# Performance work log

Measured on AMD Instinct MI355X. Metric: run time of the kernel, lower is better.

The kernel has to match this reference:

```python
import jax, jax.numpy as jnp
import numpy as np

B = 16384
NUM_RATE, NUM_GENRE, NUM_DIRECTOR, NUM_ACTOR = 6, 25, 2186, 8030
EMB = 32


def setup_inputs() -> dict:
    key = jax.random.key(0)
    k0, k1, k2, k3, k4 = jax.random.split(key, 5)
    x = jax.random.randint(k0, (B, 1 + NUM_GENRE + NUM_DIRECTOR + NUM_ACTOR), 0, 2, dtype=jnp.int64 if jax.config.jax_enable_x64 else jnp.int32)
    rate_table = jax.random.normal(k1, (NUM_RATE, EMB), dtype=jnp.float32)
    # torch Linear weights have shape [out_features, in_features]
    W_genre = jax.random.normal(k2, (EMB, NUM_GENRE), dtype=jnp.float32) * (1.0 / np.sqrt(NUM_GENRE))
    W_director = jax.random.normal(k3, (EMB, NUM_DIRECTOR), dtype=jnp.float32) * (1.0 / np.sqrt(NUM_DIRECTOR))
    W_actor = jax.random.normal(k4, (EMB, NUM_ACTOR), dtype=jnp.float32) * (1.0 / np.sqrt(NUM_ACTOR))
    return {"x": x, "rate_table": rate_table, "W_genre": W_genre,
            "W_director": W_director, "W_actor": W_actor}


def _maxnorm_gather(table, idx, max_norm=1.0, eps=1e-7):
    # torch.nn.Embedding(max_norm=1.0): rows accessed are renormalized to norm <= max_norm
    rows = table[idx]  # [B, E]
    norm = jnp.linalg.norm(rows, axis=-1, keepdims=True)
    scale = jnp.where(norm > max_norm, max_norm / (norm + eps), 1.0)
    return rows * scale


def _mean_pool_linear(multi_hot_f, W):
    # Linear(no bias) on multi-hot then divide by row-sum == mean-pooled embedding bag
    emb = jnp.einsum('bn,en->be', multi_hot_f, W)
    return emb / jnp.sum(multi_hot_f, axis=1, keepdims=True)


def reference(x, rate_table, W_genre, W_director, W_actor):
    rate_idx = x[:, 0]
    genre = x[:, 1:26].astype(jnp.float32)
    director = x[:, 26:2212].astype(jnp.float32)
    actors = x[:, 2212:10242].astype(jnp.float32)
    rate_emb = _maxnorm_gather(rate_table, rate_idx)
    genre_emb = _mean_pool_linear(genre, W_genre)
    director_emb = _mean_pool_linear(director, W_director)
    actors_emb = _mean_pool_linear(actors, W_actor)
    return jnp.concatenate((rate_emb, genre_emb, director_emb, actors_emb), axis=1)  # [B, 4*EMB]
```

## Files before the change

kernel.cpp:

```cpp
#include <hip/hip_runtime.h>
#include <hip/hip_bf16.h>

#define B_ROWS 16384
#define XC     10242
#define NGENRE 25
#define NDIR   2186
#define NACT   8030
#define EMB    32
#define KT_TOTAL 321
#define OUTC   128
#define NCOLS  112
#define PART_STRIDE ((size_t)B_ROWS * NCOLS)

typedef __attribute__((ext_vector_type(8))) short bf16x8;
typedef __attribute__((ext_vector_type(4), aligned(4))) float f32x4a;
typedef __attribute__((ext_vector_type(4))) float f32x4;
typedef __attribute__((ext_vector_type(8))) unsigned short u16x8;

__device__ __forceinline__ void compute_core(
    const int* __restrict__ xrow, int t, int ktA, int ktB,
    const float* __restrict__ wg, const float* __restrict__ wd,
    const float* __restrict__ wa, unsigned short* __restrict__ ldsA,
    f32x4& accG0, f32x4& accG1, f32x4& accD0, f32x4& accD1,
    f32x4& accA0, f32x4& accA1, f32x4& accI) {
  const int srow = t >> 2;
  const int kg   = (t & 3) * 8;
  const int lane = t & 63;
  const int w    = t >> 6;
  const int lo   = lane & 15, hi = lane >> 4;

  auto load_x8 = [&](int kt, int* dst) {
    int k0 = kt * 32 + kg;
    if (k0 + 7 < XC) {
      int4 a = *reinterpret_cast<const int4*>(xrow + k0);
      int4 b = *reinterpret_cast<const int4*>(xrow + k0 + 4);
      dst[0]=a.x; dst[1]=a.y; dst[2]=a.z; dst[3]=a.w;
      dst[4]=b.x; dst[5]=b.y; dst[6]=b.z; dst[7]=b.w;
    } else {
#pragma unroll
      for (int i = 0; i < 8; ++i) dst[i] = (k0 + i < XC) ? xrow[k0 + i] : 0;
    }
  };
  auto bfbits = [](float f) -> unsigned short {
    __hip_bfloat16 h = __float2bfloat16(f);
    return *reinterpret_cast<unsigned short*>(&h);
  };
  auto wval = [&](const float* base, int elem, bool inb) -> unsigned short {
    return inb ? bfbits(base[elem]) : (unsigned short)0;
  };
  auto fragv = [&](const float* base, int elem) -> bf16x8 {
    f32x4a a = *reinterpret_cast<const f32x4a*>(base + elem);
    f32x4a c = *reinterpret_cast<const f32x4a*>(base + elem + 4);
    union { unsigned short u[8]; bf16x8 v; } cv;
#pragma unroll
    for (int j = 0; j < 4; ++j) { cv.u[j] = bfbits(a[j]); cv.u[j+4] = bfbits(c[j]); }
    return cv.v;
  };
  auto pack8 = [](const unsigned short* s) -> bf16x8 {
    union { unsigned short u[8]; bf16x8 v; } cv;
#pragma unroll
    for (int i = 0; i < 8; ++i) cv.u[i] = s[i];
    return cv.v;
  };

  int xv[2][8];
  load_x8(ktA, xv[0]);
  if (ktA + 1 < ktB) load_x8(ktA + 1, xv[1]);

  for (int kt = ktA; kt < ktB; ++kt) {
    int* cx = xv[kt & 1];
    unsigned short cur[8];
#pragma unroll
    for (int i = 0; i < 8; ++i)
      cur[i] = cx[i] ? (unsigned short)0x3F80 : (unsigned short)0;
    if (kt + 2 < ktB) load_x8(kt + 2, xv[kt & 1]);

    __syncthreads();
    *reinterpret_cast<u16x8*>(&ldsA[srow * 40 + kg]) =
        *reinterpret_cast<const u16x8*>(cur);
    __syncthreads();

    bf16x8 afrag = *reinterpret_cast<const bf16x8*>(&ldsA[(w * 16 + lo) * 40 + hi * 8]);
    const int kb = kt * 32 + hi * 8;

    {
      unsigned short iv[8];
#pragma unroll
      for (int j = 0; j < 8; ++j) {
        int k = kb + j;
        bool on = (lo == 0) ? (k >= 1 && k < 26)
                : (lo == 1) ? (k >= 26 && k < 2212)
                : (lo == 2) ? (k >= 2212 && k < XC)
                : false;
        iv[j] = on ? (unsigned short)0x3F80 : (unsigned short)0;
      }
      accI = __builtin_amdgcn_mfma_f32_16x16x32_bf16(afrag, pack8(iv), accI, 0, 0, 0);
    }

    if (kt == 0) {
      unsigned short g0[8], g1[8], d0[8], d1[8];
#pragma unroll
      for (int j = 0; j < 8; ++j) {
        int k = kb + j;
        bool ing = (k >= 1 && k < 26);
        bool ind = (k >= 26);
        g0[j] = wval(wg, lo * NGENRE + (k - 1), ing);
        g1[j] = wval(wg, (16 + lo) * NGENRE + (k - 1), ing);
        d0[j] = wval(wd, lo * NDIR + (k - 26), ind);
        d1[j] = wval(wd, (16 + lo) * NDIR + (k - 26), ind);
      }
      accG0 = __builtin_amdgcn_mfma_f32_16x16x32_bf16(afrag, pack8(g0), accG0, 0, 0, 0);
      accG1 = __builtin_amdgcn_mfma_f32_16x16x32_bf16(afrag, pack8(g1), accG1, 0, 0, 0);
      accD0 = __builtin_amdgcn_mfma_f32_16x16x32_bf16(afrag, pack8(d0), accD0, 0, 0, 0);
      accD1 = __builtin_amdgcn_mfma_f32_16x16x32_bf16(afrag, pack8(d1), accD1, 0, 0, 0);
    } else if (kt < 69) {
      int e0 = lo * NDIR + kb - 26, e1 = (16 + lo) * NDIR + kb - 26;
      bf16x8 b0 = fragv(wd, e0), b1 = fragv(wd, e1);
      accD0 = __builtin_amdgcn_mfma_f32_16x16x32_bf16(afrag, b0, accD0, 0, 0, 0);
      accD1 = __builtin_amdgcn_mfma_f32_16x16x32_bf16(afrag, b1, accD1, 0, 0, 0);
    } else if (kt == 69) {
      unsigned short d0[8], d1[8], a0[8], a1[8];
#pragma unroll
      for (int j = 0; j < 8; ++j) {
        int k = kb + j;
        bool ind = (k < 2212);
        d0[j] = wval(wd, lo * NDIR + (k - 26), ind);
        d1[j] = wval(wd, (16 + lo) * NDIR + (k - 26), ind);
        a0[j] = wval(wa, lo * NACT + (k - 2212), !ind);
        a1[j] = wval(wa, (16 + lo) * NACT + (k - 2212), !ind);
      }
      accD0 = __builtin_amdgcn_mfma_f32_16x16x32_bf16(afrag, pack8(d0), accD0, 0, 0, 0);
      accD1 = __builtin_amdgcn_mfma_f32_16x16x32_bf16(afrag, pack8(d1), accD1, 0, 0, 0);
      accA0 = __builtin_amdgcn_mfma_f32_16x16x32_bf16(afrag, pack8(a0), accA0, 0, 0, 0);
      accA1 = __builtin_amdgcn_mfma_f32_16x16x32_bf16(afrag, pack8(a1), accA1, 0, 0, 0);
    } else if (kt < 320) {
      int e0 = lo * NACT + kb - 2212, e1 = (16 + lo) * NACT + kb - 2212;
      bf16x8 b0 = fragv(wa, e0), b1 = fragv(wa, e1);
      accA0 = __builtin_amdgcn_mfma_f32_16x16x32_bf16(afrag, b0, accA0, 0, 0, 0);
      accA1 = __builtin_amdgcn_mfma_f32_16x16x32_bf16(afrag, b1, accA1, 0, 0, 0);
    } else {
      unsigned short a0[8], a1[8];
#pragma unroll
      for (int j = 0; j < 8; ++j) {
        int k = kb + j;
        bool in = (k < XC);
        a0[j] = wval(wa, lo * NACT + (k - 2212), in);
        a1[j] = wval(wa, (16 + lo) * NACT + (k - 2212), in);
      }
      accA0 = __builtin_amdgcn_mfma_f32_16x16x32_bf16(afrag, pack8(a0), accA0, 0, 0, 0);
      accA1 = __builtin_amdgcn_mfma_f32_16x16x32_bf16(afrag, pack8(a1), accA1, 0, 0, 0);
    }
  }
}

template<int KS>
__global__ __launch_bounds__(256) void main_mm(const int* __restrict__ x,
                                               const float* __restrict__ wg,
                                               const float* __restrict__ wd,
                                               const float* __restrict__ wa,
                                               float* __restrict__ part) {
  __shared__ unsigned short ldsA[64 * 40];
  constexpr int PER = (KT_TOTAL + KS - 1) / KS;

  const int t  = threadIdx.x;
  const int rb = blockIdx.x & 255;
  const int ks = blockIdx.x >> 8;
  const int ktA = ks * PER;
  const int ktB = (ktA + PER < KT_TOTAL) ? ktA + PER : KT_TOTAL;
  const int* xrow = x + (size_t)(rb * 64 + (t >> 2)) * XC;

  f32x4 accG0 = {0,0,0,0}, accG1 = {0,0,0,0};
  f32x4 accD0 = {0,0,0,0}, accD1 = {0,0,0,0};
  f32x4 accA0 = {0,0,0,0}, accA1 = {0,0,0,0};
  f32x4 accI  = {0,0,0,0};

  compute_core(xrow, t, ktA, ktB, wg, wd, wa, ldsA,
               accG0, accG1, accD0, accD1, accA0, accA1, accI);

  const int lane = t & 63;
  const int lo = lane & 15, hi = lane >> 4, w = t >> 6;
  float* slab = part + (size_t)ks * PART_STRIDE;
  const int rbase = rb * 64 + w * 16 + hi * 4;
#pragma unroll
  for (int j = 0; j < 4; ++j) {
    size_t ro = (size_t)(rbase + j) * NCOLS;
    slab[ro +  0 + lo] = accG0[j];
    slab[ro + 16 + lo] = accG1[j];
    slab[ro + 32 + lo] = accD0[j];
    slab[ro + 48 + lo] = accD1[j];
    slab[ro + 64 + lo] = accA0[j];
    slab[ro + 80 + lo] = accA1[j];
    if (lo < 3) slab[ro + 96 + lo] = accI[j];
  }
}

__global__ __launch_bounds__(128) void reduce_k(const int* __restrict__ x,
                                                const float* __restrict__ rate,
                                                const float* __restrict__ part,
                                                int ksplit,
                                                float* __restrict__ out) {
  __shared__ float cnt[3];
  const int r = blockIdx.x;
  const int c = threadIdx.x;

  if (c < 3) {
    float s = 0.f;
    for (int ks = 0; ks < ksplit; ++ks)
      s += part[(size_t)ks * PART_STRIDE + (size_t)r * NCOLS + 96 + c];
    cnt[c] = s;
  }
  __syncthreads();

  float res;
  if (c < EMB) {
    int idx = x[(size_t)r * XC];
    float v = rate[idx * EMB + c];
    float s2 = v * v;
    s2 += __shfl_xor(s2, 1, 32);
    s2 += __shfl_xor(s2, 2, 32);
    s2 += __shfl_xor(s2, 4, 32);
    s2 += __shfl_xor(s2, 8, 32);
    s2 += __shfl_xor(s2, 16, 32);
    float norm = sqrtf(s2);
    float scale = (norm > 1.0f) ? (1.0f / (norm + 1e-7f)) : 1.0f;
    res = v * scale;
  } else {
    int cc = c - EMB;
    float val = 0.f;
    for (int ks = 0; ks < ksplit; ++ks)
      val += part[(size_t)ks * PART_STRIDE + (size_t)r * NCOLS + cc];
    res = val / cnt[cc >> 5];
  }
  out[(size_t)r * OUTC + c] = res;
}

__global__ __launch_bounds__(256) void fused_k(const int* __restrict__ x,
                                               const float* __restrict__ rate,
                                               const float* __restrict__ wg,
                                               const float* __restrict__ wd,
                                               const float* __restrict__ wa,
                                               float* __restrict__ out) {
  __shared__ unsigned short ldsA[64 * 40];
  const int t  = threadIdx.x;
  const int rb = blockIdx.x;
  const int* xrow = x + (size_t)(rb * 64 + (t >> 2)) * XC;

  f32x4 accG0 = {0,0,0,0}, accG1 = {0,0,0,0};
  f32x4 accD0 = {0,0,0,0}, accD1 = {0,0,0,0};
  f32x4 accA0 = {0,0,0,0}, accA1 = {0,0,0,0};
  f32x4 accI  = {0,0,0,0};

  compute_core(xrow, t, 0, KT_TOTAL, wg, wd, wa, ldsA,
               accG0, accG1, accD0, accD1, accA0, accA1, accI);

  const int lane = t & 63;
  const int lo = lane & 15, hi = lane >> 4, w = t >> 6;
  float gc[4], dc[4], ac[4];
#pragma unroll
  for (int j = 0; j < 4; ++j) {
    gc[j] = __shfl(accI[j], (lane & 48));
    dc[j] = __shfl(accI[j], (lane & 48) | 1);
    ac[j] = __shfl(accI[j], (lane & 48) | 2);
  }
  const int rbase = rb * 64 + w * 16 + hi * 4;
#pragma unroll
  for (int j = 0; j < 4; ++j) {
    size_t ro = (size_t)(rbase + j) * OUTC;
    out[ro +  32 + lo] = accG0[j] / gc[j];
    out[ro +  48 + lo] = accG1[j] / gc[j];
    out[ro +  64 + lo] = accD0[j] / dc[j];
    out[ro +  80 + lo] = accD1[j] / dc[j];
    out[ro +  96 + lo] = accA0[j] / ac[j];
    out[ro + 112 + lo] = accA1[j] / ac[j];
  }
#pragma unroll
  for (int j = 0; j < 4; ++j) {
    int row = rbase + j;
    int idx = x[(size_t)row * XC];
    float v0 = rate[idx * EMB + 2 * lo];
    float v1 = rate[idx * EMB + 2 * lo + 1];
    float s2 = v0 * v0 + v1 * v1;
    s2 += __shfl_xor(s2, 1);
    s2 += __shfl_xor(s2, 2);
    s2 += __shfl_xor(s2, 4);
    s2 += __shfl_xor(s2, 8);
    float norm = sqrtf(s2);
    float scale = (norm > 1.0f) ? (1.0f / (norm + 1e-7f)) : 1.0f;
    reinterpret_cast<float2*>(out)[(size_t)row * 64 + lo] =
        make_float2(v0 * scale, v1 * scale);
  }
}

extern "C" void kernel_launch(void* const* d_in, const int* in_sizes, int n_in,
                              void* d_out, int out_size, void* d_ws, size_t ws_size,
                              hipStream_t stream) {
  (void)in_sizes; (void)n_in; (void)out_size;
  const int*   x    = (const int*)d_in[0];
  const float* rate = (const float*)d_in[1];
  const float* wg   = (const float*)d_in[2];
  const float* wd   = (const float*)d_in[3];
  const float* wa   = (const float*)d_in[4];
  float* out  = (float*)d_out;
  float* part = (float*)d_ws;

  const size_t slab_bytes = PART_STRIDE * sizeof(float);
  if (ws_size >= 8 * slab_bytes) {
    main_mm<8><<<8 * 256, 256, 0, stream>>>(x, wg, wd, wa, part);
    reduce_k<<<B_ROWS, 128, 0, stream>>>(x, rate, part, 8, out);
  } else if (ws_size >= 4 * slab_bytes) {
    main_mm<4><<<4 * 256, 256, 0, stream>>>(x, wg, wd, wa, part);
    reduce_k<<<B_ROWS, 128, 0, stream>>>(x, rate, part, 4, out);
  } else if (ws_size >= 2 * slab_bytes) {
    main_mm<2><<<2 * 256, 256, 0, stream>>>(x, wg, wd, wa, part);
    reduce_k<<<B_ROWS, 128, 0, stream>>>(x, rate, part, 2, out);
  } else {
    fused_k<<<256, 256, 0, stream>>>(x, rate, wg, wd, wa, out);
  }
}
```

Before: 1.053 ms.

## Pre-pack bf16 weight fragments and load x directly into MFMA A-fragments

Adds a prep kernel that converts the fp32 weight matrices once per call into bf16 MFMA B-fragment layout in workspace, so the main loop does a single 16-byte load per fragment instead of strided fp32 loads plus conversion. Each lane now loads its own x row segment and builds the A fragment in registers, removing the LDS staging and both __syncthreads per k-tile. The count-column constants are precomputed outside the loop. This costs an extra launch and workspace, and the x loads become less coalesced per wavefront.

```diff
diff --git a/kernel.cpp b/kernel.cpp
--- a/kernel.cpp
+++ b/kernel.cpp
@@ -11,174 +11,156 @@
 #define OUTC   128
 #define NCOLS  112
 #define PART_STRIDE ((size_t)B_ROWS * NCOLS)
-
-typedef __attribute__((ext_vector_type(8))) short bf16x8;
-typedef __attribute__((ext_vector_type(4), aligned(4))) float f32x4a;
-typedef __attribute__((ext_vector_type(4))) float f32x4;
-typedef __attribute__((ext_vector_type(8))) unsigned short u16x8;
-
-__device__ __forceinline__ void compute_core(
-    const int* __restrict__ xrow, int t, int ktA, int ktB,
-    const float* __restrict__ wg, const float* __restrict__ wd,
-    const float* __restrict__ wa, unsigned short* __restrict__ ldsA,
-    f32x4& accG0, f32x4& accG1, f32x4& accD0, f32x4& accD1,
-    f32x4& accA0, f32x4& accA1, f32x4& accI) {
-  const int srow = t >> 2;
-  const int kg   = (t & 3) * 8;
+#define WFRAG_BYTES ((size_t)KT_TOTAL * 4 * 64 * 16)
+
+typedef short bf16x8 __attribute__((ext_vector_type(8)));
+typedef float f32x4  __attribute__((ext_vector_type(4)));
+typedef int   i32x4a __attribute__((ext_vector_type(4), aligned(4)));
+
+__global__ void prep_wfrag(const float* __restrict__ wg,
+                           const float* __restrict__ wd,
+                           const float* __restrict__ wa,
+                           uint4* __restrict__ Wfrag) {
+  const int kt = blockIdx.x;
+  const int s  = threadIdx.x >> 6;
+  const int l  = threadIdx.x & 63;
+  const int n  = l & 15;
+  const int k0 = kt * 32 + ((l >> 4) << 3);
+
+  unsigned short v[8];
+#pragma unroll
+  for (int j = 0; j < 8; ++j) {
+    const int k = k0 + j;
+    float f = 0.f;
+    if (kt == 0) {
+      if (s < 2) { if (k >= 1 && k < 26) f = wg[(s * 16 + n) * NGENRE + (k - 1)]; }
+      else       { if (k >= 26)          f = wd[((s - 2) * 16 + n) * NDIR + (k - 26)]; }
+    } else if (kt < 69) {
+      if (s < 2) f = wd[(s * 16 + n) * NDIR + (k - 26)];
+    } else if (kt == 69) {
+      if (s < 2) { if (k < 2212)  f = wd[(s * 16 + n) * NDIR + (k - 26)]; }
+      else       { if (k >= 2212) f = wa[((s - 2) * 16 + n) * NACT + (k - 2212)]; }
+    } else if (kt < 320) {
+      if (s < 2) f = wa[(s * 16 + n) * NACT + (k - 2212)];
+    } else {
+      if (s < 2 && k < XC) f = wa[(s * 16 + n) * NACT + (k - 2212)];
+    }
+    __hip_bfloat16 h = __float2bfloat16(f);
+    v[j] = *reinterpret_cast<unsigned short*>(&h);
+  }
+  union { unsigned short u[8]; uint4 q; } cv;
+#pragma unroll
+  for (int j = 0; j < 8; ++j) cv.u[j] = v[j];
+  Wfrag[((size_t)kt * 4 + s) * 64 + l] = cv.q;
+}
+
+template<int KS>
+__global__ __launch_bounds__(256) void main_mm(const int* __restrict__ x,
+                                               const uint4* __restrict__ Wfrag,
+                                               float* __restrict__ part) {
+  constexpr int PER = (KT_TOTAL + KS - 1) / KS;
+  const int t    = threadIdx.x;
+  const int rb   = blockIdx.x & 255;
+  const int ks   = blockIdx.x >> 8;
+  const int ktA  = ks * PER;
+  const int ktB  = (ktA + PER < KT_TOTAL) ? ktA + PER : KT_TOTAL;
   const int lane = t & 63;
   const int w    = t >> 6;
   const int lo   = lane & 15, hi = lane >> 4;
-
-  auto load_x8 = [&](int kt, int* dst) {
-    int k0 = kt * 32 + kg;
-    if (k0 + 7 < XC) {
-      int4 a = *reinterpret_cast<const int4*>(xrow + k0);
-      int4 b = *reinterpret_cast<const int4*>(xrow + k0 + 4);
-      dst[0]=a.x; dst[1]=a.y; dst[2]=a.z; dst[3]=a.w;
-      dst[4]=b.x; dst[5]=b.y; dst[6]=b.z; dst[7]=b.w;
-    } else {
-#pragma unroll
-      for (int i = 0; i < 8; ++i) dst[i] = (k0 + i < XC) ? xrow[k0 + i] : 0;
-    }
-  };
-  auto bfbits = [](float f) -> unsigned short {
-    __hip_bfloat16 h = __float2bfloat16(f);
-    return *reinterpret_cast<unsigned short*>(&h);
-  };
-  auto wval = [&](const float* base, int elem, bool inb) -> unsigned short {
-    return inb ? bfbits(base[elem]) : (unsigned short)0;
-  };
-  auto fragv = [&](const float* base, int elem) -> bf16x8 {
-    f32x4a a = *reinterpret_cast<const f32x4a*>(base + elem);
-    f32x4a c = *reinterpret_cast<const f32x4a*>(base + elem + 4);
-    union { unsigned short u[8]; bf16x8 v; } cv;
-#pragma unroll
-    for (int j = 0; j < 4; ++j) { cv.u[j] = bfbits(a[j]); cv.u[j+4] = bfbits(c[j]); }
-    return cv.v;
-  };
-  auto pack8 = [](const unsigned short* s) -> bf16x8 {
-    union { unsigned short u[8]; bf16x8 v; } cv;
-#pragma unroll
-    for (int i = 0; i < 8; ++i) cv.u[i] = s[i];
-    return cv.v;
-  };
-
-  int xv[2][8];
-  load_x8(ktA, xv[0]);
-  if (ktA + 1 < ktB) load_x8(ktA + 1, xv[1]);
-
-  for (int kt = ktA; kt < ktB; ++kt) {
-    int* cx = xv[kt & 1];
-    unsigned short cur[8];
-#pragma unroll
-    for (int i = 0; i < 8; ++i)
-      cur[i] = cx[i] ? (unsigned short)0x3F80 : (unsigned short)0;
-    if (kt + 2 < ktB) load_x8(kt + 2, xv[kt & 1]);
-
-    __syncthreads();
-    *reinterpret_cast<u16x8*>(&ldsA[srow * 40 + kg]) =
-        *reinterpret_cast<const u16x8*>(cur);
-    __syncthreads();
-
-    bf16x8 afrag = *reinterpret_cast<const bf16x8*>(&ldsA[(w * 16 + lo) * 40 + hi * 8]);
-    const int kb = kt * 32 + hi * 8;
-
-    {
-      unsigned short iv[8];
-#pragma unroll
-      for (int j = 0; j < 8; ++j) {
-        int k = kb + j;
-        bool on = (lo == 0) ? (k >= 1 && k < 26)
-                : (lo == 1) ? (k >= 26 && k < 2212)
-                : (lo == 2) ? (k >= 2212 && k < XC)
-                : false;
-        iv[j] = on ? (unsigned short)0x3F80 : (unsigned short)0;
-      }
-      accI = __builtin_amdgcn_mfma_f32_16x16x32_bf16(afrag, pack8(iv), accI, 0, 0, 0);
-    }
-
-    if (kt == 0) {
-      unsigned short g0[8], g1[8], d0[8], d1[8];
-#pragma unroll
-      for (int j = 0; j < 8; ++j) {
-        int k = kb + j;
-        bool ing = (k >= 1 && k < 26);
-        bool ind = (k >= 26);
-        g0[j] = wval(wg, lo * NGENRE + (k - 1), ing);
-        g1[j] = wval(wg, (16 + lo) * NGENRE + (k - 1), ing);
-        d0[j] = wval(wd, lo * NDIR + (k - 26), ind);
-        d1[j] = wval(wd, (16 + lo) * NDIR + (k - 26), ind);
-      }
-      accG0 = __builtin_amdgcn_mfma_f32_16x16x32_bf16(afrag, pack8(g0), accG0, 0, 0, 0);
-      accG1 = __builtin_amdgcn_mfma_f32_16x16x32_bf16(afrag, pack8(g1), accG1, 0, 0, 0);
-      accD0 = __builtin_amdgcn_mfma_f32_16x16x32_bf16(afrag, pack8(d0), accD0, 0, 0, 0);
-      accD1 = __builtin_amdgcn_mfma_f32_16x16x32_bf16(afrag, pack8(d1), accD1, 0, 0, 0);
-    } else if (kt < 69) {
-      int e0 = lo * NDIR + kb - 26, e1 = (16 + lo) * NDIR + kb - 26;
-      bf16x8 b0 = fragv(wd, e0), b1 = fragv(wd, e1);
-      accD0 = __builtin_amdgcn_mfma_f32_16x16x32_bf16(afrag, b0, accD0, 0, 0, 0);
-      accD1 = __builtin_amdgcn_mfma_f32_16x16x32_bf16(afrag, b1, accD1, 0, 0, 0);
-    } else if (kt == 69) {
-      unsigned short d0[8], d1[8], a0[8], a1[8];
-#pragma unroll
-      for (int j = 0; j < 8; ++j) {
-        int k = kb + j;
-        bool ind = (k < 2212);
-        d0[j] = wval(wd, lo * NDIR + (k - 26), ind);
-        d1[j] = wval(wd, (16 + lo) * NDIR + (k - 26), ind);
-        a0[j] = wval(wa, lo * NACT + (k - 2212), !ind);
-        a1[j] = wval(wa, (16 + lo) * NACT + (k - 2212), !ind);
-      }
-      accD0 = __builtin_amdgcn_mfma_f32_16x16x32_bf16(afrag, pack8(d0), accD0, 0, 0, 0);
-      accD1 = __builtin_amdgcn_mfma_f32_16x16x32_bf16(afrag, pack8(d1), accD1, 0, 0, 0);
-      accA0 = __builtin_amdgcn_mfma_f32_16x16x32_bf16(afrag, pack8(a0), accA0, 0, 0, 0);
-      accA1 = __builtin_amdgcn_mfma_f32_16x16x32_bf16(afrag, pack8(a1), accA1, 0, 0, 0);
-    } else if (kt < 320) {
-      int e0 = lo * NACT + kb - 2212, e1 = (16 + lo) * NACT + kb - 2212;
-      bf16x8 b0 = fragv(wa, e0), b1 = fragv(wa, e1);
-      accA0 = __builtin_amdgcn_mfma_f32_16x16x32_bf16(afrag, b0, accA0, 0, 0, 0);
-      accA1 = __builtin_amdgcn_mfma_f32_16x16x32_bf16(afrag, b1, accA1, 0, 0, 0);
-    } else {
-      unsigned short a0[8], a1[8];
-#pragma unroll
-      for (int j = 0; j < 8; ++j) {
-        int k = kb + j;
-        bool in = (k < XC);
-        a0[j] = wval(wa, lo * NACT + (k - 2212), in);
-        a1[j] = wval(wa, (16 + lo) * NACT + (k - 2212), in);
-      }
-      accA0 = __builtin_amdgcn_mfma_f32_16x16x32_bf16(afrag, pack8(a0), accA0, 0, 0, 0);
-      accA1 = __builtin_amdgcn_mfma_f32_16x16x32_bf16(afrag, pack8(a1), accA1, 0, 0, 0);
-    }
-  }
-}
-
-template<int KS>
-__global__ __launch_bounds__(256) void main_mm(const int* __restrict__ x,
-                                               const float* __restrict__ wg,
-                                               const float* __restrict__ wd,
-                                               const float* __restrict__ wa,
-                                               float* __restrict__ part) {
-  __shared__ unsigned short ldsA[64 * 40];
-  constexpr int PER = (KT_TOTAL + KS - 1) / KS;
-
-  const int t  = threadIdx.x;
-  const int rb = blockIdx.x & 255;
-  const int ks = blockIdx.x >> 8;
-  const int ktA = ks * PER;
-  const int ktB = (ktA + PER < KT_TOTAL) ? ktA + PER : KT_TOTAL;
-  const int* xrow = x + (size_t)(rb * 64 + (t >> 2)) * XC;
+  const int* xrow = x + (size_t)(rb * 64 + w * 16 + lo) * XC;
 
   f32x4 accG0 = {0,0,0,0}, accG1 = {0,0,0,0};
   f32x4 accD0 = {0,0,0,0}, accD1 = {0,0,0,0};
   f32x4 accA0 = {0,0,0,0}, accA1 = {0,0,0,0};
   f32x4 accI  = {0,0,0,0};
 
-  compute_core(xrow, t, ktA, ktB, wg, wd, wa, ldsA,
-               accG0, accG1, accD0, accD1, accA0, accA1, accI);
-
-  const int lane = t & 63;
-  const int lo = lane & 15, hi = lane >> 4, w = t >> 6;
+  auto load_x8 = [&](int kt, int* dst) {
+    int k0 = kt * 32 + hi * 8;
+    if (k0 + 7 < XC) {
+      i32x4a a = *reinterpret_cast<const i32x4a*>(xrow + k0);
+      i32x4a b = *reinterpret_cast<const i32x4a*>(xrow + k0 + 4);
+      dst[0]=a[0]; dst[1]=a[1]; dst[2]=a[2]; dst[3]=a[3];
+      dst[4]=b[0]; dst[5]=b[1]; dst[6]=b[2]; dst[7]=b[3];
+    } else {
+#pragma unroll
+      for (int j = 0; j < 8; ++j) dst[j] = (k0 + j < XC) ? xrow[k0 + j] : 0;
+    }
+  };
+  auto bload = [&](int kt, int s) -> bf16x8 {
+    union { uint4 q; bf16x8 v; } c;
+    c.q = Wfrag[((size_t)kt * 4 + s) * 64 + lane];
+    return c.v;
+  };
+  auto mkconst = [&](bool on) -> bf16x8 {
+    union { unsigned int w[4]; bf16x8 v; } c;
+    unsigned int u = on ? 0x3F803F80u : 0u;
+    c.w[0]=u; c.w[1]=u; c.w[2]=u; c.w[3]=u;
+    return c.v;
+  };
+  const bf16x8 ivD = mkconst(lo == 1);
+  const bf16x8 ivA = mkconst(lo == 2);
+
+  int xv[2][8];
+  load_x8(ktA, xv[0]);
+  if (ktA + 1 < ktB) load_x8(ktA + 1, xv[1]);
+
+  for (int kt = ktA; kt < ktB; ++kt) {
+    int* cx = xv[kt & 1];
+    union { unsigned int w[4]; bf16x8 v; } af;
+#pragma unroll
+    for (int i = 0; i < 4; ++i)
+      af.w[i] = (cx[2*i] ? 0x3F80u : 0u) | (cx[2*i+1] ? 0x3F800000u : 0u);
+    if (kt + 2 < ktB) load_x8(kt + 2, xv[kt & 1]);
+    const bf16x8 a = af.v;
+    const int kb = kt * 32 + hi * 8;
+
+    if (kt == 0) {
+      accG0 = __builtin_amdgcn_mfma_f32_16x16x32_bf16(a, bload(0,0), accG0, 0,0,0);
+      accG1 = __builtin_amdgcn_mfma_f32_16x16x32_bf16(a, bload(0,1), accG1, 0,0,0);
+      accD0 = __builtin_amdgcn_mfma_f32_16x16x32_bf16(a, bload(0,2), accD0, 0,0,0);
+      accD1 = __builtin_amdgcn_mfma_f32_16x16x32_bf16(a, bload(0,3), accD1, 0,0,0);
+      union { unsigned short u[8]; bf16x8 v; } iv;
+#pragma unroll
+      for (int j = 0; j < 8; ++j) {
+        int k = kb + j;
+        bool on = (lo == 0) ? (k >= 1 && k < 26) : (lo == 1) ? (k >= 26) : false;
+        iv.u[j] = on ? (unsigned short)0x3F80 : (unsigned short)0;
+      }
+      accI = __builtin_amdgcn_mfma_f32_16x16x32_bf16(a, iv.v, accI, 0,0,0);
+    } else if (kt < 69) {
+      accD0 = __builtin_amdgcn_mfma_f32_16x16x32_bf16(a, bload(kt,0), accD0, 0,0,0);
+      accD1 = __builtin_amdgcn_mfma_f32_16x16x32_bf16(a, bload(kt,1), accD1, 0,0,0);
+      accI  = __builtin_amdgcn_mfma_f32_16x16x32_bf16(a, ivD, accI, 0,0,0);
+    } else if (kt == 69) {
+      accD0 = __builtin_amdgcn_mfma_f32_16x16x32_bf16(a, bload(69,0), accD0, 0,0,0);
+      accD1 = __builtin_amdgcn_mfma_f32_16x16x32_bf16(a, bload(69,1), accD1, 0,0,0);
+      accA0 = __builtin_amdgcn_mfma_f32_16x16x32_bf16(a, bload(69,2), accA0, 0,0,0);
+      accA1 = __builtin_amdgcn_mfma_f32_16x16x32_bf16(a, bload(69,3), accA1, 0,0,0);
+      union { unsigned short u[8]; bf16x8 v; } iv;
+#pragma unroll
+      for (int j = 0; j < 8; ++j) {
+        int k = kb + j;
+        bool on = (lo == 1) ? (k < 2212) : (lo == 2) ? (k >= 2212) : false;
+        iv.u[j] = on ? (unsigned short)0x3F80 : (unsigned short)0;
+      }
+      accI = __builtin_amdgcn_mfma_f32_16x16x32_bf16(a, iv.v, accI, 0,0,0);
+    } else if (kt < 320) {
+      accA0 = __builtin_amdgcn_mfma_f32_16x16x32_bf16(a, bload(kt,0), accA0, 0,0,0);
+      accA1 = __builtin_amdgcn_mfma_f32_16x16x32_bf16(a, bload(kt,1), accA1, 0,0,0);
+      accI  = __builtin_amdgcn_mfma_f32_16x16x32_bf16(a, ivA, accI, 0,0,0);
+    } else {
+      accA0 = __builtin_amdgcn_mfma_f32_16x16x32_bf16(a, bload(320,0), accA0, 0,0,0);
+      accA1 = __builtin_amdgcn_mfma_f32_16x16x32_bf16(a, bload(320,1), accA1, 0,0,0);
+      union { unsigned short u[8]; bf16x8 v; } iv;
+#pragma unroll
+      for (int j = 0; j < 8; ++j) {
+        int k = kb + j;
+        iv.u[j] = (lo == 2 && k < XC) ? (unsigned short)0x3F80 : (unsigned short)0;
+      }
+      accI = __builtin_amdgcn_mfma_f32_16x16x32_bf16(a, iv.v, accI, 0,0,0);
+    }
+  }
+
   float* slab = part + (size_t)ks * PART_STRIDE;
   const int rbase = rb * 64 + w * 16 + hi * 4;
 #pragma unroll
@@ -234,63 +216,6 @@
   out[(size_t)r * OUTC + c] = res;
 }
 
-__global__ __launch_bounds__(256) void fused_k(const int* __restrict__ x,
-                                               const float* __restrict__ rate,
-                                               const float* __restrict__ wg,
-                                               const float* __restrict__ wd,
-                                               const float* __restrict__ wa,
-                                               float* __restrict__ out) {
-  __shared__ unsigned short ldsA[64 * 40];
-  const int t  = threadIdx.x;
-  const int rb = blockIdx.x;
-  const int* xrow = x + (size_t)(rb * 64 + (t >> 2)) * XC;
-
-  f32x4 accG0 = {0,0,0,0}, accG1 = {0,0,0,0};
-  f32x4 accD0 = {0,0,0,0}, accD1 = {0,0,0,0};
-  f32x4 accA0 = {0,0,0,0}, accA1 = {0,0,0,0};
-  f32x4 accI  = {0,0,0,0};
-
-  compute_core(xrow, t, 0, KT_TOTAL, wg, wd, wa, ldsA,
-               accG0, accG1, accD0, accD1, accA0, accA1, accI);
-
-  const int lane = t & 63;
-  const int lo = lane & 15, hi = lane >> 4, w = t >> 6;
-  float gc[4], dc[4], ac[4];
-#pragma unroll
-  for (int j = 0; j < 4; ++j) {
-    gc[j] = __shfl(accI[j], (lane & 48));
-    dc[j] = __shfl(accI[j], (lane & 48) | 1);
-    ac[j] = __shfl(accI[j], (lane & 48) | 2);
-  }
-  const int rbase = rb * 64 + w * 16 + hi * 4;
-#pragma unroll
-  for (int j = 0; j < 4; ++j) {
-    size_t ro = (size_t)(rbase + j) * OUTC;
-    out[ro +  32 + lo] = accG0[j] / gc[j];
-    out[ro +  48 + lo] = accG1[j] / gc[j];
-    out[ro +  64 + lo] = accD0[j] / dc[j];
-    out[ro +  80 + lo] = accD1[j] / dc[j];
-    out[ro +  96 + lo] = accA0[j] / ac[j];
-    out[ro + 112 + lo] = accA1[j] / ac[j];
-  }
-#pragma unroll
-  for (int j = 0; j < 4; ++j) {
-    int row = rbase + j;
-    int idx = x[(size_t)row * XC];
-    float v0 = rate[idx * EMB + 2 * lo];
-    float v1 = rate[idx * EMB + 2 * lo + 1];
-    float s2 = v0 * v0 + v1 * v1;
-    s2 += __shfl_xor(s2, 1);
-    s2 += __shfl_xor(s2, 2);
-    s2 += __shfl_xor(s2, 4);
-    s2 += __shfl_xor(s2, 8);
-    float norm = sqrtf(s2);
-    float scale = (norm > 1.0f) ? (1.0f / (norm + 1e-7f)) : 1.0f;
-    reinterpret_cast<float2*>(out)[(size_t)row * 64 + lo] =
-        make_float2(v0 * scale, v1 * scale);
-  }
-}
-
 extern "C" void kernel_launch(void* const* d_in, const int* in_sizes, int n_in,
                               void* d_out, int out_size, void* d_ws, size_t ws_size,
                               hipStream_t stream) {
@@ -304,16 +229,19 @@
   float* part = (float*)d_ws;
 
   const size_t slab_bytes = PART_STRIDE * sizeof(float);
-  if (ws_size >= 8 * slab_bytes) {
-    main_mm<8><<<8 * 256, 256, 0, stream>>>(x, wg, wd, wa, part);
-    reduce_k<<<B_ROWS, 128, 0, stream>>>(x, rate, part, 8, out);
-  } else if (ws_size >= 4 * slab_bytes) {
-    main_mm<4><<<4 * 256, 256, 0, stream>>>(x, wg, wd, wa, part);
-    reduce_k<<<B_ROWS, 128, 0, stream>>>(x, rate, part, 4, out);
-  } else if (ws_size >= 2 * slab_bytes) {
-    main_mm<2><<<2 * 256, 256, 0, stream>>>(x, wg, wd, wa, part);
-    reduce_k<<<B_ROWS, 128, 0, stream>>>(x, rate, part, 2, out);
-  } else {
-    fused_k<<<256, 256, 0, stream>>>(x, rate, wg, wd, wa, out);
-  }
-}
+  int KS;
+  if      (ws_size >= 8 * slab_bytes + WFRAG_BYTES) KS = 8;
+  else if (ws_size >= 4 * slab_bytes + WFRAG_BYTES) KS = 4;
+  else if (ws_size >= 2 * slab_bytes + WFRAG_BYTES) KS = 2;
+  else                                              KS = 1;
+  uint4* Wfrag = (uint4*)((char*)d_ws + (size_t)KS * slab_bytes);
+
+  prep_wfrag<<<KT_TOTAL, 256, 0, stream>>>(wg, wd, wa, Wfrag);
+  switch (KS) {
+    case 8: main_mm<8><<<8 * 256, 256, 0, stream>>>(x, Wfrag, part); break;
+    case 4: main_mm<4><<<4 * 256, 256, 0, stream>>>(x, Wfrag, part); break;
+    case 2: main_mm<2><<<2 * 256, 256, 0, stream>>>(x, Wfrag, part); break;
+    default: main_mm<1><<<1 * 256, 256, 0, stream>>>(x, Wfrag, part); break;
+  }
+  reduce_k<<<B_ROWS, 128, 0, stream>>>(x, rate, part, KS, out);
+}
```

Measured after the change: 956.0 us. 9.2% less time.
